# Optimization experiments

Measured on AMD Instinct MI355X. Metric: run time of the kernel, lower is better.

The kernel has to match this reference:

```python
import jax, jax.numpy as jnp
import numpy as np

PI = np.pi
N_QUBITS = 10
DIM = 2 ** N_QUBITS
HALF = 2 ** (N_QUBITS - 1)
BATCH = 8192


def _bit_table(n):
    # [2^n, n] bools, qubit 0 = most significant bit (matches dec2bin)
    rows = np.arange(2 ** n)
    return ((rows[:, None] >> np.arange(n - 1, -1, -1)[None, :]) & 1).astype(bool)


def _cnot_perm(n, c_bit, t_bit):
    # CNOT as an index permutation: flip target bit where control bit is set.
    idx = np.arange(2 ** n)
    cmask = 1 << (n - 1 - c_bit)
    tmask = 1 << (n - 1 - t_bit)
    return np.where((idx & cmask) != 0, idx ^ tmask, idx)


def _ry2(theta):
    a = theta / 2
    c = jnp.cos(a).astype(jnp.complex64)
    s = jnp.sin(a).astype(jnp.complex64)
    return jnp.stack([c, -s, s, c]).reshape(2, 2)


def _rx2(theta):
    a = theta / 2
    c = jnp.cos(a).astype(jnp.complex64)
    s = jnp.sin(a).astype(jnp.complex64)
    return jnp.stack([c, -1j * s, -1j * s, c]).reshape(2, 2)


def _rz2(theta):
    a = theta / 2
    e_m = jnp.exp(-1j * a).astype(jnp.complex64)
    e_p = jnp.exp(1j * a).astype(jnp.complex64)
    z = jnp.zeros((), jnp.complex64)
    return jnp.stack([e_m, z, z, e_p]).reshape(2, 2)


def setup_inputs() -> dict:
    key = jax.random.key(0)
    k1, k2 = jax.random.split(key)
    inputs = jax.random.normal(k1, (BATCH, N_QUBITS), dtype=jnp.float32)
    weight = jax.random.normal(k2, (3 + 2 * N_QUBITS,), dtype=jnp.float32)
    # entangle_matrix: product of chained CNOT(i, i+1) gates -> real 0/1 permutation matrix
    E = np.eye(DIM, dtype=np.float32)
    for i in range(N_QUBITS - 1):
        perm = _cnot_perm(N_QUBITS, i, i + 1)
        P = np.zeros((DIM, DIM), dtype=np.float32)
        P[perm, np.arange(DIM)] = 1.0
        E = P @ E
    return {"inputs": inputs, "weight": weight, "entangle_matrix": jnp.asarray(E)}


def reference(inputs, weight, entangle_matrix):
    n = N_QUBITS
    B = inputs.shape[0]
    # torch: if inputs.max() > 1: inputs = arctan(inputs)
    inputs = jnp.where(inputs.max() > 1.0, jnp.arctan(inputs), inputs)

    # ---- Encoder: |psi> = kron_q (e^{-i a_q/2}, e^{+i a_q/2}) / sqrt(2)
    angles = (2.0 * PI) * inputs                                   # [B, n]
    v = jnp.stack([jnp.exp(-1j * angles / 2), jnp.exp(1j * angles / 2)], axis=-1)
    v = v / np.float32(np.sqrt(2.0))                               # [B, n, 2]
    vec = jnp.ones((B, 1), jnp.complex64)
    for q in range(n):                                             # qubit 0 = MSB
        vec = (vec[:, :, None] * v[:, q, None, :]).reshape(B, -1)  # [B, 2^(q+1)]

    # ---- higher order encoding: CNOT . Rz(t, 2pi*x_c*x_t) . CNOT for each c<t
    bits = _bit_table(n)                                           # [2^n, n]
    for c in range(n):
        for t in range(c + 1, n):
            perm = _cnot_perm(n, c, t)
            vec = vec[:, perm]
            ang = inputs[:, c] * inputs[:, t] * (2.0 * PI)          # [B]
            e_m = jnp.exp(-1j * ang / 2)[:, None]
            e_p = jnp.exp(1j * ang / 2)[:, None]
            vec = vec * jnp.where(bits[None, :, t], e_m, e_p)
            vec = vec[:, perm]

    # ---- trainable rotation layer: kron_q Rx(w_q*2pi) @ Rz(w_{n+q}*2pi)
    R = jnp.ones((1, 1), jnp.complex64)
    for q in range(n):
        R = jnp.kron(R, _rx2(weight[3 + q] * 2 * PI) @ _rz2(weight[3 + n + q] * 2 * PI))
    E = entangle_matrix.astype(jnp.complex64)
    M = E @ R @ E                                                  # [2^n, 2^n]
    vec = vec @ M.T                                                # tensordot(vec, M, ([-1],[-1]))

    # ---- final rotation on qubit 0 (note: original uses ry-form for all three)
    Rf = _ry2(weight[2] * 2 * PI) @ (_ry2(weight[1] * 2 * PI) @ _ry2(weight[0] * 2 * PI))
    vec = jnp.einsum('ij,bja->bia', Rf, vec.reshape(B, 2, HALF)).reshape(B, -1)

    # ---- measurement: <Z_0> style difference of probabilities
    probs = vec.real ** 2 + vec.imag ** 2
    return probs[:, HALF:].sum(-1) - probs[:, :HALF].sum(-1)
```

## Files before the change

### kernel.cpp

```cpp
#include <hip/hip_runtime.h>
#include <math.h>

#define NQ 10
#define BATCHN 8192


__global__ __launch_bounds__(256) void prep_kernel(const float* __restrict__ in,
                                                   int n,
                                                   const float* __restrict__ w,
                                                   int* __restrict__ flags,
                                                   float* __restrict__ gtab) {
    __shared__ int bf;
    if (threadIdx.x == 0) bf = 0;
    __syncthreads();
    const int tid = blockIdx.x * 256 + threadIdx.x;
    bool pred = false;
    for (int i = tid; i < n; i += 64 * 256) pred |= (in[i] > 1.0f);
    if (__any(pred) && (threadIdx.x & 63) == 0) atomicOr(&bf, 1);
    __syncthreads();
    if (threadIdx.x == 0) flags[blockIdx.x] = bf;

    if (blockIdx.x == 0 && threadIdx.x == 0) {
        const float sw  = w[0] + w[1] + w[2];
        const float cb  = __builtin_amdgcn_cosf(sw);
        const float sb  = __builtin_amdgcn_sinf(sw);
        const float st0 = __builtin_amdgcn_sinf(w[3]);
        gtab[0] = 0.5f * cb * st0;
        gtab[1] = 0.5f * sb;
        gtab[2] = w[13];
        gtab[3] = w[14];
    }
}

__global__ __launch_bounds__(256) void expect_kernel(const float* __restrict__ in,
                                                     const int* __restrict__ flags,
                                                     const float* __restrict__ G,
                                                     float* __restrict__ out) {
    __shared__ float xs[256 * NQ];
    const int base = blockIdx.x * (256 * NQ);
    for (int i = threadIdx.x; i < 256 * NQ; i += 256) xs[i] = in[base + i];

    const int lane = threadIdx.x & 63;
    const bool anyflag = __any(flags[lane] != 0);

    const float g0 = G[0], g1 = G[1], l0 = G[2], l1 = G[3];

    __syncthreads();

    float x[NQ];
#pragma unroll
    for (int q = 0; q < NQ; ++q) x[q] = xs[threadIdx.x * NQ + q];
    if (anyflag) {
#pragma unroll
        for (int q = 0; q < NQ; ++q) x[q] = atanf(x[q]);
    }

    const float mp = x[0] + x[1], mm = x[0] - x[1];
    const float np_ = x[0] + x[2], nm = x[0] - x[2];

    float Kmp = 1.0f, Kmm = 1.0f, Knp = 1.0f, Knm = 1.0f;
#pragma unroll
    for (int t = 3; t < NQ; ++t) {
        Kmp *= __builtin_amdgcn_cosf(mp * x[t]);
        Kmm *= __builtin_amdgcn_cosf(mm * x[t]);
        Knp *= __builtin_amdgcn_cosf(np_ * x[t]);
        Knm *= __builtin_amdgcn_cosf(nm * x[t]);
    }

    const float t1 = __builtin_amdgcn_sinf(mp + l0) * __builtin_amdgcn_cosf(mp * x[2]) * Kmp
                   + __builtin_amdgcn_sinf(mm + l0) * __builtin_amdgcn_cosf(mm * x[2]) * Kmm;
    const float t2 = __builtin_amdgcn_cosf(np_ + l0) * __builtin_amdgcn_cosf(np_ * x[1] - l1) * Knp
                   + __builtin_amdgcn_cosf(nm + l0) * __builtin_amdgcn_cosf(nm * x[1] - l1) * Knm;

    const int b = blockIdx.x * 256 + threadIdx.x;
    out[b] = fmaf(-g0, t1, g1 * t2);
}

extern "C" void kernel_launch(void* const* d_in, const int* in_sizes, int n_in,
                              void* d_out, int out_size, void* d_ws, size_t ws_size,
                              hipStream_t stream) {
    const float* inputs = (const float*)d_in[0];
    const float* weight = (const float*)d_in[1];
    float* out   = (float*)d_out;
    int*   flags = (int*)d_ws;
    float* gtab  = (float*)d_ws + 64;

    prep_kernel<<<64, 256, 0, stream>>>(inputs, BATCHN * NQ, weight, flags, gtab);
    expect_kernel<<<BATCHN / 256, 256, 0, stream>>>(inputs, flags, gtab, out);
}
```

Before: 63.18 us.

## Fuse global max check and weight prep into single expectation kernel

Merges the prep kernel (global max>1 check and weight-derived constants) into the main kernel. Each of the 32 blocks now scans the whole 320KB input with float4 loads to compute the global max redundantly, stashing its own slice into shared memory along the way, and computes the weight constants per thread. This removes one kernel launch and the workspace round trip. In exchange every block reads the full input (32x redundant reads, mostly L2 hits).

New measurement: 79.71 us. 26.2% more time.

```diff
diff --git a/kernel.cpp b/kernel.cpp
--- a/kernel.cpp
+++ b/kernel.cpp
@@ -3,49 +3,36 @@
 
 #define NQ 10
 #define BATCHN 8192
+#define NF4 ((BATCHN * NQ) / 4)
+#define BLK4 (256 * NQ / 4)
 
 
-__global__ __launch_bounds__(256) void prep_kernel(const float* __restrict__ in,
-                                                   int n,
-                                                   const float* __restrict__ w,
-                                                   int* __restrict__ flags,
-                                                   float* __restrict__ gtab) {
+__global__ __launch_bounds__(256) void fused_kernel(const float* __restrict__ in,
+                                                    const float* __restrict__ w,
+                                                    float* __restrict__ out) {
+    __shared__ float xs[256 * NQ];
     __shared__ int bf;
     if (threadIdx.x == 0) bf = 0;
     __syncthreads();
-    const int tid = blockIdx.x * 256 + threadIdx.x;
-    bool pred = false;
-    for (int i = tid; i < n; i += 64 * 256) pred |= (in[i] > 1.0f);
-    if (__any(pred) && (threadIdx.x & 63) == 0) atomicOr(&bf, 1);
-    __syncthreads();
-    if (threadIdx.x == 0) flags[blockIdx.x] = bf;
 
-    if (blockIdx.x == 0 && threadIdx.x == 0) {
-        const float sw  = w[0] + w[1] + w[2];
-        const float cb  = __builtin_amdgcn_cosf(sw);
-        const float sb  = __builtin_amdgcn_sinf(sw);
-        const float st0 = __builtin_amdgcn_sinf(w[3]);
-        gtab[0] = 0.5f * cb * st0;
-        gtab[1] = 0.5f * sb;
-        gtab[2] = w[13];
-        gtab[3] = w[14];
+    const float4* __restrict__ in4 = (const float4*)in;
+    const int base4 = blockIdx.x * BLK4;
+    float mx = -1.0f;
+    for (int i = threadIdx.x; i < NF4; i += 256) {
+        const float4 v = in4[i];
+        mx = fmaxf(mx, fmaxf(fmaxf(v.x, v.y), fmaxf(v.z, v.w)));
+        const unsigned d = (unsigned)(i - base4);
+        if (d < (unsigned)BLK4) ((float4*)xs)[d] = v;
     }
-}
+    if (__any(mx > 1.0f) && (threadIdx.x & 63) == 0) atomicOr(&bf, 1);
 
-__global__ __launch_bounds__(256) void expect_kernel(const float* __restrict__ in,
-                                                     const int* __restrict__ flags,
-                                                     const float* __restrict__ G,
-                                                     float* __restrict__ out) {
-    __shared__ float xs[256 * NQ];
-    const int base = blockIdx.x * (256 * NQ);
-    for (int i = threadIdx.x; i < 256 * NQ; i += 256) xs[i] = in[base + i];
-
-    const int lane = threadIdx.x & 63;
-    const bool anyflag = __any(flags[lane] != 0);
-
-    const float g0 = G[0], g1 = G[1], l0 = G[2], l1 = G[3];
+    const float sw = w[0] + w[1] + w[2];
+    const float g0 = 0.5f * __builtin_amdgcn_cosf(sw) * __builtin_amdgcn_sinf(w[3]);
+    const float g1 = 0.5f * __builtin_amdgcn_sinf(sw);
+    const float l0 = w[13], l1 = w[14];
 
     __syncthreads();
+    const bool anyflag = (bf != 0);
 
     float x[NQ];
 #pragma unroll
@@ -55,7 +42,7 @@
         for (int q = 0; q < NQ; ++q) x[q] = atanf(x[q]);
     }
 
-    const float mp = x[0] + x[1], mm = x[0] - x[1];
+    const float mp  = x[0] + x[1], mm = x[0] - x[1];
     const float np_ = x[0] + x[2], nm = x[0] - x[2];
 
     float Kmp = 1.0f, Kmm = 1.0f, Knp = 1.0f, Knm = 1.0f;
@@ -72,8 +59,7 @@
     const float t2 = __builtin_amdgcn_cosf(np_ + l0) * __builtin_amdgcn_cosf(np_ * x[1] - l1) * Knp
                    + __builtin_amdgcn_cosf(nm + l0) * __builtin_amdgcn_cosf(nm * x[1] - l1) * Knm;
 
-    const int b = blockIdx.x * 256 + threadIdx.x;
-    out[b] = fmaf(-g0, t1, g1 * t2);
+    out[blockIdx.x * 256 + threadIdx.x] = fmaf(-g0, t1, g1 * t2);
 }
 
 extern "C" void kernel_launch(void* const* d_in, const int* in_sizes, int n_in,
@@ -81,10 +67,7 @@
                               hipStream_t stream) {
     const float* inputs = (const float*)d_in[0];
     const float* weight = (const float*)d_in[1];
-    float* out   = (float*)d_out;
-    int*   flags = (int*)d_ws;
-    float* gtab  = (float*)d_ws + 64;
+    float* out = (float*)d_out;
 
-    prep_kernel<<<64, 256, 0, stream>>>(inputs, BATCHN * NQ, weight, flags, gtab);
-    expect_kernel<<<BATCHN / 256, 256, 0, stream>>>(inputs, flags, gtab, out);
+    fused_kernel<<<BATCHN / 256, 256, 0, stream>>>(inputs, weight, out);
 }
```
